# Kernel tuning notes

Hardware: AMD Instinct MI355X
Metric: run time of the kernel (lower is better)

The kernel has to match this reference:

```python
import jax, jax.numpy as jnp
import numpy as np

N_NODES = 100000
N_EDGES = 1600000
N_GRAPHS = 64
IN_DIM = 256
OUT_DIM = 512
H1 = OUT_DIM // 4   # 128
H2 = OUT_DIM // 2   # 256


def glorot(key, shape):
    lim = float(np.sqrt(6.0 / (shape[0] + shape[1])))
    return jax.random.uniform(key, shape, jnp.float32, -lim, lim)


def setup_inputs() -> dict:
    key = jax.random.key(0)
    ks = jax.random.split(key, 8)
    x = jax.random.normal(ks[0], (N_NODES, IN_DIM), jnp.float32)
    edge_index = jax.random.randint(ks[1], (2, N_EDGES), 0, N_NODES, jnp.int64)
    batch = jnp.sort(jax.random.randint(ks[2], (N_NODES,), 0, N_GRAPHS, jnp.int64))
    return {
        'x': x,
        'edge_index': edge_index,
        'batch': batch,
        'W1': glorot(ks[3], (IN_DIM, H1)),
        'b1': jnp.zeros((H1,), jnp.float32),
        'W2': glorot(ks[4], (H1, H2)),
        'b2': jnp.zeros((H2,), jnp.float32),
        'fc_W': glorot(ks[5], (H2, OUT_DIM)),
        'fc_b': jnp.zeros((OUT_DIM,), jnp.float32),
    }


def gcn_conv(x, W, b, src, dst, n_nodes):
    # PyG GCNConv (default): add self-loops, sym-normalized aggregation of XW + bias
    h = x @ W                                   # [N, F_out] transform first (cheaper gather)
    ones = jnp.ones((src.shape[0],), h.dtype)
    deg = jax.ops.segment_sum(ones, dst, num_segments=n_nodes)  # includes self-loops
    dinv = jax.lax.rsqrt(jnp.maximum(deg, 1.0))
    norm = dinv[src] * dinv[dst]                # [E]
    msg = h[src] * norm[:, None]                # gather + scale
    out = jax.ops.segment_sum(msg, dst, num_segments=n_nodes)   # scatter-add
    return out + b


def reference(x, edge_index, batch, W1, b1, W2, b2, fc_W, fc_b):
    n = x.shape[0]
    loops = jnp.arange(n, dtype=edge_index.dtype)
    src = jnp.concatenate([edge_index[0], loops])
    dst = jnp.concatenate([edge_index[1], loops])

    h = jax.nn.relu(gcn_conv(x, W1, b1, src, dst, n))   # dropout = identity (eval)
    h = jax.nn.relu(gcn_conv(h, W2, b2, src, dst, n))

    # global_mean_pool over batch ids
    sums = jax.ops.segment_sum(h, batch, num_segments=N_GRAPHS)
    cnts = jax.ops.segment_sum(jnp.ones((n,), h.dtype), batch, num_segments=N_GRAPHS)
    pooled = sums / jnp.maximum(cnts, 1.0)[:, None]     # [B, H2]

    return jax.nn.relu(pooled @ fc_W + fc_b)            # [B, OUT_DIM]
```

## Files before the change

### kernel.cpp

```cpp
#include <hip/hip_runtime.h>
#include <hip/hip_bf16.h>
#include <cstdint>

#define N_NODES 100000
#define N_EDGES 1600000
#define N_GRAPHS 64
#define IN_DIM 256
#define HD1 128
#define HD2 256
#define OUT_DIM 512

#define NBUCK 196
#define NBLK  196
#define EPB   8192

typedef __bf16 bf16x8 __attribute__((ext_vector_type(8)));
typedef float f32x4 __attribute__((ext_vector_type(4)));

static __device__ __forceinline__ float bflo(uint32_t v) { return __uint_as_float(v << 16); }
static __device__ __forceinline__ float bfhi(uint32_t v) { return __uint_as_float(v & 0xffff0000u); }
static __device__ __forceinline__ uint32_t f2bf_bits(float f) {
    uint32_t u = __float_as_uint(f);
    return (u + 0x7fffu + ((u >> 16) & 1u)) >> 16;
}
static __device__ __forceinline__ uint32_t packbf(float a, float b) {
    return f2bf_bits(a) | (f2bf_bits(b) << 16);
}
static __device__ __forceinline__ float bf2f(uint16_t b) { return __uint_as_float(((uint32_t)b) << 16); }

static __device__ __forceinline__ void gl_lds16(const void* g, void* l) {
    __builtin_amdgcn_global_load_lds((const __attribute__((address_space(1))) uint32_t*)g,
                                     (__attribute__((address_space(3))) uint32_t*)l, 16, 0, 0);
}

__global__ void k_probe(const uint32_t* __restrict__ xw, const int* __restrict__ ei,
                        int* __restrict__ flags) {
    if (threadIdx.x != 0 || blockIdx.x != 0) return;
    int mid = 0;
    for (int i = 0; i < 64; i++) {
        uint32_t f = (xw[i] >> 23) & 0xFF;
        if (f >= 64 && f < 200) mid++;
    }
    flags[0] = (mid < 32) ? 1 : 0;
    int nz = 0;
    for (int i = 0; i < 64; i++) if (ei[2 * i + 1] != 0) nz++;
    flags[1] = (nz == 0) ? 1 : 0;
}

static __device__ __forceinline__ int ld_idx(const int* p, int i, int sh) { return p[i << sh]; }
static __device__ __forceinline__ float ld_f(const void* p, int i, int isbf) {
    return isbf ? bf2f(((const uint16_t*)p)[i]) : ((const float*)p)[i];
}

__global__ __launch_bounds__(256) void k_prep(const void* __restrict__ W1, const void* __restrict__ W2,
                                              const void* __restrict__ fcW, const void* __restrict__ b1,
                                              const void* __restrict__ b2, const void* __restrict__ fcb,
                                              uint16_t* __restrict__ W1F, uint16_t* __restrict__ W2F,
                                              uint16_t* __restrict__ fcWc, uint16_t* __restrict__ bc1,
                                              uint16_t* __restrict__ bc2, uint16_t* __restrict__ fcbc,
                                              const int* __restrict__ flags) {
    int i = blockIdx.x * 256 + threadIdx.x;
    int isbf = flags[0];
    if (i < 32768) {
        int j = i & 7, l = (i >> 3) & 63, nt = (i >> 9) & 1, ks = (i >> 10) & 7, n0g = (i >> 13) & 3;
        int k = ks * 32 + (l >> 4) * 8 + j;
        int n = n0g * 32 + nt * 16 + (l & 15);
        W1F[i] = (uint16_t)f2bf_bits(ld_f(W1, k * HD1 + n, isbf));
    } else if (i < 65536) {
        int j2 = i - 32768;
        int j = j2 & 7, l = (j2 >> 3) & 63, nt = (j2 >> 9) & 1, ks = (j2 >> 10) & 3, n0g = (j2 >> 12) & 7;
        int k = ks * 32 + (l >> 4) * 8 + j;
        int n = n0g * 32 + nt * 16 + (l & 15);
        W2F[j2] = (uint16_t)f2bf_bits(ld_f(W2, k * HD2 + n, isbf));
    } else if (i < 196608) {
        int j = i - 65536;
        fcWc[j] = (uint16_t)f2bf_bits(ld_f(fcW, j, isbf));
    } else if (i < 196736) {
        bc1[i - 196608] = (uint16_t)f2bf_bits(ld_f(b1, i - 196608, isbf));
    } else if (i < 196992) {
        bc2[i - 196736] = (uint16_t)f2bf_bits(ld_f(b2, i - 196736, isbf));
    } else if (i < 197504) {
        fcbc[i - 196992] = (uint16_t)f2bf_bits(ld_f(fcb, i - 196992, isbf));
    }
}


__global__ __launch_bounds__(256) void k_hist(const int* __restrict__ ei, int* __restrict__ bh,
                                              const int* __restrict__ flags) {
    __shared__ int h[NBUCK];
    int t = threadIdx.x, blk = blockIdx.x;
    if (t < NBUCK) h[t] = 0;
    __syncthreads();
    int sh = flags[1];
    int base = blk * EPB;
#pragma unroll
    for (int k = 0; k < EPB / 256; k++) {
        int e = base + k * 256 + t;
        if (e < N_EDGES) atomicAdd(&h[ld_idx(ei, N_EDGES + e, sh) >> 9], 1);
    }
    __syncthreads();
    if (t < NBUCK) bh[blk * NBUCK + t] = h[t];
}

__global__ __launch_bounds__(256) void k_colscan(const int* __restrict__ bh, int* __restrict__ bhoff,
                                                 int* __restrict__ bucket_cnt) {
    __shared__ int s[256];
    int b = blockIdx.x, t = threadIdx.x;
    int v = (t < NBLK) ? bh[t * NBUCK + b] : 0;
    s[t] = v; __syncthreads();
    for (int off = 1; off < 256; off <<= 1) {
        int x = (t >= off) ? s[t - off] : 0;
        __syncthreads();
        s[t] += x;
        __syncthreads();
    }
    if (t < NBLK) bhoff[t * NBUCK + b] = s[t] - v;
    if (t == 255) bucket_cnt[b] = s[255];
}

__global__ __launch_bounds__(256) void k_bscan(const int* __restrict__ bucket_cnt,
                                               int* __restrict__ bucket_base,
                                               int* __restrict__ row_ptr) {
    __shared__ int s[256];
    int t = threadIdx.x;
    int v = (t < NBUCK) ? bucket_cnt[t] : 0;
    s[t] = v; __syncthreads();
    for (int off = 1; off < 256; off <<= 1) {
        int x = (t >= off) ? s[t - off] : 0;
        __syncthreads();
        s[t] += x;
        __syncthreads();
    }
    if (t < NBUCK) bucket_base[t] = s[t] - v;
    if (t == NBUCK - 1) { bucket_base[NBUCK] = s[t]; row_ptr[N_NODES] = s[t]; }
}

__global__ __launch_bounds__(256) void k_part(const int* __restrict__ ei,
                                              const int* __restrict__ bucket_base,
                                              const int* __restrict__ bhoff,
                                              int* __restrict__ tmp,
                                              const int* __restrict__ flags) {
    __shared__ int cur[NBUCK];
    int t = threadIdx.x, blk = blockIdx.x;
    if (t < NBUCK) cur[t] = bucket_base[t] + bhoff[blk * NBUCK + t];
    __syncthreads();
    int sh = flags[1];
    int base = blk * EPB;
#pragma unroll
    for (int k = 0; k < EPB / 256; k++) {
        int e = base + k * 256 + t;
        if (e < N_EDGES) {
            int s = ld_idx(ei, e, sh), d = ld_idx(ei, N_EDGES + e, sh);
            int pos = atomicAdd(&cur[d >> 9], 1);
            tmp[pos] = (s << 9) | (d & 511);
        }
    }
}

__global__ __launch_bounds__(256) void k_bsort(const int* __restrict__ tmp,
                                               const int* __restrict__ bucket_base,
                                               int* __restrict__ csr_src,
                                               int* __restrict__ row_ptr,
                                               float* __restrict__ dinv) {
    __shared__ int h[512], a[512], c[512];
    int b = blockIdx.x, t = threadIdx.x;
    int beg = bucket_base[b], end = bucket_base[b + 1];
    h[t] = 0; h[t + 256] = 0;
    __syncthreads();
    for (int i = beg + t; i < end; i += 256) atomicAdd(&h[tmp[i] & 511], 1);
    __syncthreads();
    a[t] = h[t]; a[t + 256] = h[t + 256];
    __syncthreads();
    for (int off = 1; off < 512; off <<= 1) {
        int x0 = (t >= off) ? a[t - off] : 0;
        int x1 = ((t + 256) >= off) ? a[t + 256 - off] : 0;
        __syncthreads();
        a[t] += x0; a[t + 256] += x1;
        __syncthreads();
    }
#pragma unroll
    for (int u = 0; u < 2; u++) {
        int i = t + u * 256;
        int node = (b << 9) + i;
        int ex = a[i] - h[i];
        if (node < N_NODES) {
            row_ptr[node] = beg + ex;
            dinv[node] = rsqrtf((float)(h[i] + 1));
        }
        c[i] = ex;
    }
    __syncthreads();
    for (int i = beg + t; i < end; i += 256) {
        int e = tmp[i];
        int pos = atomicAdd(&c[e & 511], 1);
        csr_src[beg + pos] = e >> 9;
    }
}

#define GCNT_CHUNK 8
__global__ __launch_bounds__(256) void k_gcnt(const int* __restrict__ bat, int* __restrict__ gcnt,
                                              const int* __restrict__ flags) {
    __shared__ int h[N_GRAPHS];
    int t = threadIdx.x;
    if (t < N_GRAPHS) h[t] = 0;
    __syncthreads();
    int sh = flags[1];
    int base = (blockIdx.x * 256 + t) * GCNT_CHUNK;
    int cur = -1, run = 0;
#pragma unroll
    for (int u = 0; u < GCNT_CHUNK; u++) {
        int i = base + u;
        if (i < N_NODES) {
            int g = ld_idx(bat, i, sh);
            if (g == cur) run++;
            else { if (run) atomicAdd(&h[cur], run); cur = g; run = 1; }
        }
    }
    if (run) atomicAdd(&h[cur], run);
    __syncthreads();
    if (t < N_GRAPHS) { int v = h[t]; if (v) atomicAdd(&gcnt[t], v); }
}


__global__ __launch_bounds__(256) void k_gemm1(const void* __restrict__ Ain,
                                               const uint16_t* __restrict__ BF,
                                               uint16_t* __restrict__ C,
                                               const int* __restrict__ flags) {
    __shared__ __align__(16) uint16_t As[64 * 256];
    const int M = N_NODES, N = HD1;
    int isbf = flags[0];
    int t = threadIdx.x;
    int wave = t >> 6, lane = t & 63;
    int quad = lane >> 4, l16 = lane & 15;
    int m0 = blockIdx.x * 64;
    int n0 = wave * 32;

    bf16x8 Bf[8][2];
#pragma unroll
    for (int ks = 0; ks < 8; ks++)
#pragma unroll
        for (int nt = 0; nt < 2; nt++)
            Bf[ks][nt] = *(const bf16x8*)(BF + ((((wave * 8 + ks) * 2 + nt) << 6) + lane) * 8);

    if (isbf) {
        const uint8_t* Xb = (const uint8_t*)Ain;
#pragma unroll
        for (int i = 0; i < 8; i++) {
            int o = (i * 256 + t) * 16;
            int r = o >> 9, c = o & 511;
            int rg = m0 + r; if (rg >= M) rg = M - 1;
            gl_lds16(Xb + (size_t)rg * 512 + (c ^ ((r & 7) << 4)), (uint8_t*)As + o);
        }
    } else {
        const float* Xf = (const float*)Ain;
#pragma unroll
        for (int i = 0; i < 8; i++) {
            int o = (i * 256 + t) * 16;
            int r = o >> 9, c = (o & 511) ^ ((r & 7) << 4);
            int rg = m0 + r; if (rg >= M) rg = M - 1;
            const float* p = Xf + (size_t)rg * 256 + (c >> 1);
            f32x4 f0 = *(const f32x4*)p, f1 = *(const f32x4*)(p + 4);
            union { uint16_t u[8]; bf16x8 v; } rr;
#pragma unroll
            for (int j = 0; j < 4; j++) {
                rr.u[j]     = (uint16_t)f2bf_bits(f0[j]);
                rr.u[4 + j] = (uint16_t)f2bf_bits(f1[j]);
            }
            *(bf16x8*)((uint8_t*)As + o) = rr.v;
        }
    }
    __syncthreads();

    f32x4 acc[4][2];
#pragma unroll
    for (int a = 0; a < 4; a++)
#pragma unroll
        for (int b = 0; b < 2; b++) acc[a][b] = f32x4{0.f, 0.f, 0.f, 0.f};

#pragma unroll
    for (int ks = 0; ks < 8; ks++) {
        bf16x8 af[4];
#pragma unroll
        for (int mt = 0; mt < 4; mt++) {
            int r = mt * 16 + l16;
            int cb = (ks * 64 + quad * 16) ^ ((r & 7) << 4);
            af[mt] = *(const bf16x8*)((const uint8_t*)As + r * 512 + cb);
        }
#pragma unroll
        for (int mt = 0; mt < 4; mt++)
#pragma unroll
            for (int nt = 0; nt < 2; nt++)
                acc[mt][nt] = __builtin_amdgcn_mfma_f32_16x16x32_bf16(af[mt], Bf[ks][nt], acc[mt][nt], 0, 0, 0);
    }

#pragma unroll
    for (int mt = 0; mt < 4; mt++)
#pragma unroll
        for (int reg = 0; reg < 4; reg++) {
            int row = m0 + mt * 16 + quad * 4 + reg;
            if (row < M)
#pragma unroll
                for (int nt = 0; nt < 2; nt++)
                    C[row * N + n0 + nt * 16 + l16] = (uint16_t)f2bf_bits(acc[mt][nt][reg]);
        }
}


template <int WITH_BIAS_RELU>
__global__ __launch_bounds__(256) void k_agg(const uint16_t* __restrict__ Yin, uint16_t* __restrict__ Yout,
                                             const int* __restrict__ row_ptr, const int* __restrict__ csr_src,
                                             const float* __restrict__ dinv, const uint16_t* __restrict__ bias) {
    int node = blockIdx.x * 4 + (threadIdx.x >> 6);
    int l = threadIdx.x & 63;
    const uint32_t* Y32 = (const uint32_t*)Yin;

    float wd = dinv[node];
    uint32_t v = Y32[(size_t)node * 64 + l];
    float a0 = wd * bflo(v), a1 = wd * bfhi(v);

    int e0 = row_ptr[node], e1 = row_ptr[node + 1];
    for (int cb = e0; cb < e1; cb += 64) {
        int cnt = e1 - cb; if (cnt > 64) cnt = 64;
        int my_src = 0; uint32_t my_w = 0;
        if (l < cnt) { my_src = csr_src[cb + l]; my_w = __float_as_uint(dinv[my_src]); }
        int rounds = (cnt + 15) >> 4;
        for (int r = 0; r < rounds; r++) {
            int jb = r * 16;
            uint32_t vv[16];
#pragma unroll
            for (int t = 0; t < 16; t++) {
                int s = __builtin_amdgcn_readlane(my_src, jb + t);
                vv[t] = Y32[(size_t)s * 64 + l];
            }
#pragma unroll
            for (int t = 0; t < 16; t++) {
                float w = __uint_as_float(__builtin_amdgcn_readlane(my_w, jb + t));
                a0 += w * bflo(vv[t]);
                a1 += w * bfhi(vv[t]);
            }
        }
    }
    a0 *= wd; a1 *= wd;
    if (WITH_BIAS_RELU) {
        a0 = fmaxf(a0 + bf2f(bias[2 * l]), 0.f);
        a1 = fmaxf(a1 + bf2f(bias[2 * l + 1]), 0.f);
    }
    ((uint32_t*)Yout)[(size_t)node * 64 + l] = packbf(a0, a1);
}


__global__ __launch_bounds__(512) void k_gemm2_pool(const uint16_t* __restrict__ A,
                                                    const uint16_t* __restrict__ BF,
                                                    const uint16_t* __restrict__ bias,
                                                    const int* __restrict__ bat,
                                                    const int* __restrict__ flags,
                                                    float* __restrict__ pooled) {
    __shared__ __align__(16) uint16_t As[64 * 128];
    const int M = N_NODES;
    int t = threadIdx.x;
    int wave = t >> 6, lane = t & 63;
    int quad = lane >> 4, l16 = lane & 15;
    int m0 = blockIdx.x * 64;
    int n0 = wave * 32;

    bf16x8 Bf[4][2];
#pragma unroll
    for (int ks = 0; ks < 4; ks++)
#pragma unroll
        for (int nt = 0; nt < 2; nt++)
            Bf[ks][nt] = *(const bf16x8*)(BF + ((((wave * 4 + ks) * 2 + nt) << 6) + lane) * 8);

#pragma unroll
    for (int i = 0; i < 2; i++) {
        int o = (i * 512 + t) * 16;
        int r = o >> 8, c = o & 255;
        int rg = m0 + r; if (rg >= M) rg = M - 1;
        gl_lds16((const uint8_t*)A + (size_t)rg * 256 + (c ^ ((r & 7) << 4)), (uint8_t*)As + o);
    }
    __syncthreads();

    f32x4 acc[4][2];
#pragma unroll
    for (int a = 0; a < 4; a++)
#pragma unroll
        for (int b = 0; b < 2; b++) acc[a][b] = f32x4{0.f, 0.f, 0.f, 0.f};

#pragma unroll
    for (int ks = 0; ks < 4; ks++) {
        bf16x8 af[4];
#pragma unroll
        for (int mt = 0; mt < 4; mt++) {
            int r = mt * 16 + l16;
            int cb = (ks * 64 + quad * 16) ^ ((r & 7) << 4);
            af[mt] = *(const bf16x8*)((const uint8_t*)As + r * 256 + cb);
        }
#pragma unroll
        for (int mt = 0; mt < 4; mt++)
#pragma unroll
            for (int nt = 0; nt < 2; nt++)
                acc[mt][nt] = __builtin_amdgcn_mfma_f32_16x16x32_bf16(af[mt], Bf[ks][nt], acc[mt][nt], 0, 0, 0);
    }

    int sh = flags[1];
    float bv[2];
#pragma unroll
    for (int nt = 0; nt < 2; nt++) bv[nt] = bf2f(bias[n0 + nt * 16 + l16]);

    int last = m0 + 63 < M ? m0 + 63 : M - 1;
    int gfirst = ld_idx(bat, m0, sh);
    int glast  = ld_idx(bat, last, sh);
    if ((m0 + 63 < M) && gfirst == glast) {
#pragma unroll
        for (int nt = 0; nt < 2; nt++) {
            float s = 0.f;
#pragma unroll
            for (int mt = 0; mt < 4; mt++)
#pragma unroll
                for (int reg = 0; reg < 4; reg++)
                    s += fmaxf(acc[mt][nt][reg] + bv[nt], 0.f);
            s += __shfl_xor(s, 16);
            s += __shfl_xor(s, 32);
            if (quad == 0)
                atomicAdd(&pooled[gfirst * HD2 + n0 + nt * 16 + l16], s);
        }
    } else {
#pragma unroll
        for (int mt = 0; mt < 4; mt++) {
#pragma unroll
            for (int reg = 0; reg < 4; reg++) {
                int row = m0 + mt * 16 + quad * 4 + reg;
                if (row < M) {
                    int g = ld_idx(bat, row, sh);
#pragma unroll
                    for (int nt = 0; nt < 2; nt++)
                        atomicAdd(&pooled[g * HD2 + n0 + nt * 16 + l16],
                                  fmaxf(acc[mt][nt][reg] + bv[nt], 0.f));
                }
            }
        }
    }
}


__global__ __launch_bounds__(512) void k_final(const float* __restrict__ pooled, const int* __restrict__ gcnt,
                                               const uint16_t* __restrict__ fcWc, const uint16_t* __restrict__ fcbc,
                                               void* __restrict__ out, const int* __restrict__ flags) {
    __shared__ float pm[HD2];
    int g = blockIdx.x, t = threadIdx.x;
    if (t < HD2) pm[t] = pooled[g * HD2 + t] / fmaxf((float)gcnt[g], 1.0f);
    __syncthreads();
    float acc = bf2f(fcbc[t]);
    for (int k = 0; k < HD2; k++) acc = fmaf(pm[k], bf2f(fcWc[k * OUT_DIM + t]), acc);
    acc = fmaxf(acc, 0.f);
    if (flags[0]) ((uint16_t*)out)[g * OUT_DIM + t] = (uint16_t)f2bf_bits(acc);
    else          ((float*)out)[g * OUT_DIM + t] = acc;
}


extern "C" void kernel_launch(void* const* d_in, const int* in_sizes, int n_in,
                              void* d_out, int out_size, void* d_ws, size_t ws_size,
                              hipStream_t stream) {
    const void* x   = d_in[0];
    const int*  ei  = (const int*)d_in[1];
    const int*  bat = (const int*)d_in[2];
    const void* W1  = d_in[3];
    const void* b1  = d_in[4];
    const void* W2  = d_in[5];
    const void* b2  = d_in[6];
    const void* fcW = d_in[7];
    const void* fcb = d_in[8];

    char* ws = (char*)d_ws;
    size_t off = 0;
    auto alloc = [&](size_t bytes) -> void* {
        void* p = ws + off;
        off += (bytes + 255) & ~(size_t)255;
        return p;
    };
    uint16_t* buf0 = (uint16_t*)alloc((size_t)N_NODES * HD1 * 2);
    uint16_t* Hb   = (uint16_t*)alloc((size_t)N_NODES * HD1 * 2);
    int*   row_ptr = (int*)alloc((N_NODES + 1) * 4);
    int*   csr_src = (int*)alloc((size_t)N_EDGES * 4);
    int*   tmp     = (int*)alloc((size_t)N_EDGES * 4);
    int*   bh      = (int*)alloc(NBLK * NBUCK * 4);
    int*   bhoff   = (int*)alloc(NBLK * NBUCK * 4);
    int*   bucket_cnt  = (int*)alloc(NBUCK * 4);
    int*   bucket_base = (int*)alloc((NBUCK + 1) * 4);
    float* dinv    = (float*)alloc(N_NODES * 4);
    int*   gcnt    = (int*)alloc(N_GRAPHS * 4);
    float* pooled  = (float*)alloc(N_GRAPHS * HD2 * 4);
    uint16_t* W1T  = (uint16_t*)alloc(IN_DIM * HD1 * 2);
    uint16_t* W2T  = (uint16_t*)alloc(HD1 * HD2 * 2);
    uint16_t* bc1  = (uint16_t*)alloc(HD1 * 2);
    uint16_t* bc2  = (uint16_t*)alloc(HD2 * 2);
    uint16_t* fcWc = (uint16_t*)alloc(HD2 * OUT_DIM * 2);
    uint16_t* fcbc = (uint16_t*)alloc(OUT_DIM * 2);
    int*   flags   = (int*)alloc(64 * 4);

    uint16_t* Y1 = buf0;
    uint16_t* Zb = buf0;

    hipMemsetAsync(gcnt, 0, N_GRAPHS * 4, stream);
    hipMemsetAsync(pooled, 0, N_GRAPHS * HD2 * 4, stream);

    k_probe<<<1, 64, 0, stream>>>((const uint32_t*)x, ei, flags);

    k_prep<<<(197504 + 255) / 256, 256, 0, stream>>>(W1, W2, fcW, b1, b2, fcb,
                                                     W1T, W2T, fcWc, bc1, bc2, fcbc, flags);

    k_hist<<<NBLK, 256, 0, stream>>>(ei, bh, flags);
    k_colscan<<<NBUCK, 256, 0, stream>>>(bh, bhoff, bucket_cnt);
    k_bscan<<<1, 256, 0, stream>>>(bucket_cnt, bucket_base, row_ptr);
    k_part<<<NBLK, 256, 0, stream>>>(ei, bucket_base, bhoff, tmp, flags);
    k_bsort<<<NBUCK, 256, 0, stream>>>(tmp, bucket_base, csr_src, row_ptr, dinv);

    k_gcnt<<<(N_NODES + 256 * GCNT_CHUNK - 1) / (256 * GCNT_CHUNK), 256, 0, stream>>>(bat, gcnt, flags);

    k_gemm1<<<(N_NODES + 63) / 64, 256, 0, stream>>>(x, W1T, Y1, flags);
    k_agg<1><<<N_NODES / 4, 256, 0, stream>>>(Y1, Hb, row_ptr, csr_src, dinv, bc1);

    k_agg<0><<<N_NODES / 4, 256, 0, stream>>>(Hb, Zb, row_ptr, csr_src, dinv, nullptr);
    k_gemm2_pool<<<(N_NODES + 63) / 64, 512, 0, stream>>>(Zb, W2T, bc2, bat, flags, pooled);

    k_final<<<N_GRAPHS, 512, 0, stream>>>(pooled, gcnt, fcWc, fcbc, d_out, flags);
}
```

Baseline: 417.8 us.

## Pack source index and degree weight per edge; process four nodes per wave

Adds a pass that stores each CSR edge as an (src, dinv[src]) int2, so the aggregation kernels no longer do a dependent dinv gather per edge. The aggregation now has each wave loop over four nodes and read edges in groups of 8 through scalar (readfirstlane) loads instead of cooperative 64-lane loads plus readlane. This trims launch count and the index-load dependency chain. In exchange it adds an extra kernel, 12.8MB of extra edge traffic, and less memory-level parallelism per wave (8 outstanding gathers instead of 16).

```diff
diff --git a/kernel.cpp b/kernel.cpp
--- a/kernel.cpp
+++ b/kernel.cpp
@@ -197,6 +197,16 @@
     }
 }
 
+__global__ __launch_bounds__(256) void k_wpack(const int* __restrict__ csr_src,
+                                               const float* __restrict__ dinv,
+                                               int2* __restrict__ csr_sw) {
+    int e = blockIdx.x * 256 + threadIdx.x;
+    if (e < N_EDGES) {
+        int s = csr_src[e];
+        csr_sw[e] = make_int2(s, __float_as_int(dinv[s]));
+    }
+}
+
 #define GCNT_CHUNK 8
 __global__ __launch_bounds__(256) void k_gcnt(const int* __restrict__ bat, int* __restrict__ gcnt,
                                               const int* __restrict__ flags) {
@@ -308,44 +318,49 @@
 
 template <int WITH_BIAS_RELU>
 __global__ __launch_bounds__(256) void k_agg(const uint16_t* __restrict__ Yin, uint16_t* __restrict__ Yout,
-                                             const int* __restrict__ row_ptr, const int* __restrict__ csr_src,
+                                             const int* __restrict__ row_ptr, const int2* __restrict__ csr_sw,
                                              const float* __restrict__ dinv, const uint16_t* __restrict__ bias) {
-    int node = blockIdx.x * 4 + (threadIdx.x >> 6);
     int l = threadIdx.x & 63;
+    int wid = (blockIdx.x << 2) | (threadIdx.x >> 6);
     const uint32_t* Y32 = (const uint32_t*)Yin;
-
-    float wd = dinv[node];
-    uint32_t v = Y32[(size_t)node * 64 + l];
-    float a0 = wd * bflo(v), a1 = wd * bfhi(v);
-
-    int e0 = row_ptr[node], e1 = row_ptr[node + 1];
-    for (int cb = e0; cb < e1; cb += 64) {
-        int cnt = e1 - cb; if (cnt > 64) cnt = 64;
-        int my_src = 0; uint32_t my_w = 0;
-        if (l < cnt) { my_src = csr_src[cb + l]; my_w = __float_as_uint(dinv[my_src]); }
-        int rounds = (cnt + 15) >> 4;
-        for (int r = 0; r < rounds; r++) {
-            int jb = r * 16;
-            uint32_t vv[16];
-#pragma unroll
-            for (int t = 0; t < 16; t++) {
-                int s = __builtin_amdgcn_readlane(my_src, jb + t);
+    float b0 = 0.f, b1 = 0.f;
+    if (WITH_BIAS_RELU) { b0 = bf2f(bias[2 * l]); b1 = bf2f(bias[2 * l + 1]); }
+    int nbeg = __builtin_amdgcn_readfirstlane(wid * 4);
+
+#pragma unroll 1
+    for (int node = nbeg; node < nbeg + 4; node++) {
+        int e0 = __builtin_amdgcn_readfirstlane(row_ptr[node]);
+        int e1 = __builtin_amdgcn_readfirstlane(row_ptr[node + 1]);
+        float wd = dinv[node];
+        uint32_t v = Y32[(size_t)node * 64 + l];
+        float a0 = wd * bflo(v), a1 = wd * bfhi(v);
+
+        for (int e = e0; e < e1; e += 8) {
+            uint32_t vv[8];
+            float    ww[8];
+#pragma unroll
+            for (int t = 0; t < 8; t++) {
+                int idx = (e + t < e1) ? e + t : e1 - 1;
+                int2 sw = csr_sw[idx];
+                int   s = __builtin_amdgcn_readfirstlane(sw.x);
+                float w = __uint_as_float((uint32_t)__builtin_amdgcn_readfirstlane(sw.y));
+                ww[t] = (e + t < e1) ? w : 0.f;
                 vv[t] = Y32[(size_t)s * 64 + l];
             }
 #pragma unroll
-            for (int t = 0; t < 16; t++) {
-                float w = __uint_as_float(__builtin_amdgcn_readlane(my_w, jb + t));
-                a0 += w * bflo(vv[t]);
-                a1 += w * bfhi(vv[t]);
+            for (int t = 0; t < 8; t++) {
+                a0 += ww[t] * bflo(vv[t]);
+                a1 += ww[t] * bfhi(vv[t]);
             }
         }
-    }
-    a0 *= wd; a1 *= wd;
-    if (WITH_BIAS_RELU) {
-        a0 = fmaxf(a0 + bf2f(bias[2 * l]), 0.f);
-        a1 = fmaxf(a1 + bf2f(bias[2 * l + 1]), 0.f);
-    }
-    ((uint32_t*)Yout)[(size_t)node * 64 + l] = packbf(a0, a1);
+
+        a0 *= wd; a1 *= wd;
+        if (WITH_BIAS_RELU) {
+            a0 = fmaxf(a0 + b0, 0.f);
+            a1 = fmaxf(a1 + b1, 0.f);
+        }
+        ((uint32_t*)Yout)[(size_t)node * 64 + l] = packbf(a0, a1);
+    }
 }
 
 
@@ -481,6 +496,7 @@
     uint16_t* Hb   = (uint16_t*)alloc((size_t)N_NODES * HD1 * 2);
     int*   row_ptr = (int*)alloc((N_NODES + 1) * 4);
     int*   csr_src = (int*)alloc((size_t)N_EDGES * 4);
+    int2*  csr_sw  = (int2*)alloc((size_t)N_EDGES * 8);
     int*   tmp     = (int*)alloc((size_t)N_EDGES * 4);
     int*   bh      = (int*)alloc(NBLK * NBUCK * 4);
     int*   bhoff   = (int*)alloc(NBLK * NBUCK * 4);
@@ -513,13 +529,14 @@
     k_bscan<<<1, 256, 0, stream>>>(bucket_cnt, bucket_base, row_ptr);
     k_part<<<NBLK, 256, 0, stream>>>(ei, bucket_base, bhoff, tmp, flags);
     k_bsort<<<NBUCK, 256, 0, stream>>>(tmp, bucket_base, csr_src, row_ptr, dinv);
+    k_wpack<<<N_EDGES / 256, 256, 0, stream>>>(csr_src, dinv, csr_sw);
 
     k_gcnt<<<(N_NODES + 256 * GCNT_CHUNK - 1) / (256 * GCNT_CHUNK), 256, 0, stream>>>(bat, gcnt, flags);
 
     k_gemm1<<<(N_NODES + 63) / 64, 256, 0, stream>>>(x, W1T, Y1, flags);
-    k_agg<1><<<N_NODES / 4, 256, 0, stream>>>(Y1, Hb, row_ptr, csr_src, dinv, bc1);
-
-    k_agg<0><<<N_NODES / 4, 256, 0, stream>>>(Hb, Zb, row_ptr, csr_src, dinv, nullptr);
+    k_agg<1><<<N_NODES / 16, 256, 0, stream>>>(Y1, Hb, row_ptr, csr_sw, dinv, bc1);
+
+    k_agg<0><<<N_NODES / 16, 256, 0, stream>>>(Hb, Zb, row_ptr, csr_sw, dinv, nullptr);
     k_gemm2_pool<<<(N_NODES + 63) / 64, 512, 0, stream>>>(Zb, W2T, bc2, bat, flags, pooled);
 
     k_final<<<N_GRAPHS, 512, 0, stream>>>(pooled, gcnt, fcWc, fcbc, d_out, flags);
```

Result: slower. 438.7 us (+5.0%).

## Fuse second-layer neighbor aggregation into the GEMM2 pooling kernel

Applied to the files above, without the earlier changes.

The second sparse aggregation moves from a standalone kernel into k_gemm2_pool. Each wave gathers and normalizes neighbor rows for 8 nodes and writes the bf16 result straight into the swizzled LDS tile that feeds the MFMA GEMM. This removes one kernel launch and the write and re-read of the intermediate 100000x128 activation. In exchange, the GEMM block now spends its time on latency-bound gathers, with lower occupancy at 512 threads, and can no longer overlap the tile load asynchronously.

```diff
diff --git a/kernel.cpp b/kernel.cpp
--- a/kernel.cpp
+++ b/kernel.cpp
@@ -349,10 +349,13 @@
 }
 
 
-__global__ __launch_bounds__(512) void k_gemm2_pool(const uint16_t* __restrict__ A,
+__global__ __launch_bounds__(512) void k_gemm2_pool(const uint16_t* __restrict__ Hb,
                                                     const uint16_t* __restrict__ BF,
                                                     const uint16_t* __restrict__ bias,
                                                     const int* __restrict__ bat,
+                                                    const int* __restrict__ row_ptr,
+                                                    const int* __restrict__ csr_src,
+                                                    const float* __restrict__ dinv,
                                                     const int* __restrict__ flags,
                                                     float* __restrict__ pooled) {
     __shared__ __align__(16) uint16_t As[64 * 128];
@@ -370,12 +373,41 @@
         for (int nt = 0; nt < 2; nt++)
             Bf[ks][nt] = *(const bf16x8*)(BF + ((((wave * 4 + ks) * 2 + nt) << 6) + lane) * 8);
 
-#pragma unroll
-    for (int i = 0; i < 2; i++) {
-        int o = (i * 512 + t) * 16;
-        int r = o >> 8, c = o & 255;
-        int rg = m0 + r; if (rg >= M) rg = M - 1;
-        gl_lds16((const uint8_t*)A + (size_t)rg * 256 + (c ^ ((r & 7) << 4)), (uint8_t*)As + o);
+    const uint32_t* Y32 = (const uint32_t*)Hb;
+#pragma unroll 1
+    for (int u = 0; u < 8; u++) {
+        int node = m0 + wave * 8 + u;
+        float a0 = 0.f, a1 = 0.f;
+        if (node < M) {
+            float wd = dinv[node];
+            uint32_t v = Y32[(size_t)node * 64 + lane];
+            a0 = wd * bflo(v); a1 = wd * bfhi(v);
+            int e0 = row_ptr[node], e1 = row_ptr[node + 1];
+            for (int cb = e0; cb < e1; cb += 64) {
+                int cnt = e1 - cb; if (cnt > 64) cnt = 64;
+                int my_src = 0; uint32_t my_w = 0;
+                if (lane < cnt) { my_src = csr_src[cb + lane]; my_w = __float_as_uint(dinv[my_src]); }
+                int rounds = (cnt + 15) >> 4;
+                for (int r = 0; r < rounds; r++) {
+                    int jb = r * 16;
+                    uint32_t vv[16];
+#pragma unroll
+                    for (int t2 = 0; t2 < 16; t2++) {
+                        int s = __builtin_amdgcn_readlane(my_src, jb + t2);
+                        vv[t2] = Y32[(size_t)s * 64 + lane];
+                    }
+#pragma unroll
+                    for (int t2 = 0; t2 < 16; t2++) {
+                        float w = __uint_as_float(__builtin_amdgcn_readlane(my_w, jb + t2));
+                        a0 += w * bflo(vv[t2]);
+                        a1 += w * bfhi(vv[t2]);
+                    }
+                }
+            }
+            a0 *= wd; a1 *= wd;
+        }
+        int r = wave * 8 + u;
+        ((uint32_t*)As)[r * 64 + (lane ^ ((r & 7) << 2))] = packbf(a0, a1);
     }
     __syncthreads();
 
@@ -477,7 +509,7 @@
         off += (bytes + 255) & ~(size_t)255;
         return p;
     };
-    uint16_t* buf0 = (uint16_t*)alloc((size_t)N_NODES * HD1 * 2);
+    uint16_t* Y1   = (uint16_t*)alloc((size_t)N_NODES * HD1 * 2);
     uint16_t* Hb   = (uint16_t*)alloc((size_t)N_NODES * HD1 * 2);
     int*   row_ptr = (int*)alloc((N_NODES + 1) * 4);
     int*   csr_src = (int*)alloc((size_t)N_EDGES * 4);
@@ -497,9 +529,6 @@
     uint16_t* fcbc = (uint16_t*)alloc(OUT_DIM * 2);
     int*   flags   = (int*)alloc(64 * 4);
 
-    uint16_t* Y1 = buf0;
-    uint16_t* Zb = buf0;
-
     hipMemsetAsync(gcnt, 0, N_GRAPHS * 4, stream);
     hipMemsetAsync(pooled, 0, N_GRAPHS * HD2 * 4, stream);
 
@@ -519,8 +548,8 @@
     k_gemm1<<<(N_NODES + 63) / 64, 256, 0, stream>>>(x, W1T, Y1, flags);
     k_agg<1><<<N_NODES / 4, 256, 0, stream>>>(Y1, Hb, row_ptr, csr_src, dinv, bc1);
 
-    k_agg<0><<<N_NODES / 4, 256, 0, stream>>>(Hb, Zb, row_ptr, csr_src, dinv, nullptr);
-    k_gemm2_pool<<<(N_NODES + 63) / 64, 512, 0, stream>>>(Zb, W2T, bc2, bat, flags, pooled);
+    k_gemm2_pool<<<(N_NODES + 63) / 64, 512, 0, stream>>>(Hb, W2T, bc2, bat,
+                                                          row_ptr, csr_src, dinv, flags, pooled);
 
     k_final<<<N_GRAPHS, 512, 0, stream>>>(pooled, gcnt, fcWc, fcbc, d_out, flags);
 }
```

After: 419.4 us. Within noise of the previous version (+0.4%).

## Merge independent prep, histogram, bucket sort, gemm1 and graph-count kernels via block-range dispatch

Applied to the files above, without the earlier changes.

Independent kernels are fused into combined launches that dispatch on block index: weight prep with the edge histogram, and bucket sort, the first GEMM and graph counting into one kernel. This removes launch gaps and lets independent work overlap on the GPU instead of serialising. The cost is that the merged kernel uses the GEMM's larger LDS footprint and register pressure for every block, which may reduce occupancy for the lighter sort and count blocks.

```diff
diff --git a/kernel.cpp b/kernel.cpp
--- a/kernel.cpp
+++ b/kernel.cpp
@@ -14,6 +14,11 @@
 #define NBLK  196
 #define EPB   8192
 
+#define GB1   1563
+#define GCNT_CHUNK 8
+#define GCNT_BLKS 49
+#define PREP_BLKS 772
+
 typedef __bf16 bf16x8 __attribute__((ext_vector_type(8)));
 typedef float f32x4 __attribute__((ext_vector_type(4)));
 
@@ -52,55 +57,55 @@
     return isbf ? bf2f(((const uint16_t*)p)[i]) : ((const float*)p)[i];
 }
 
-__global__ __launch_bounds__(256) void k_prep(const void* __restrict__ W1, const void* __restrict__ W2,
-                                              const void* __restrict__ fcW, const void* __restrict__ b1,
-                                              const void* __restrict__ b2, const void* __restrict__ fcb,
-                                              uint16_t* __restrict__ W1F, uint16_t* __restrict__ W2F,
-                                              uint16_t* __restrict__ fcWc, uint16_t* __restrict__ bc1,
-                                              uint16_t* __restrict__ bc2, uint16_t* __restrict__ fcbc,
-                                              const int* __restrict__ flags) {
-    int i = blockIdx.x * 256 + threadIdx.x;
-    int isbf = flags[0];
-    if (i < 32768) {
-        int j = i & 7, l = (i >> 3) & 63, nt = (i >> 9) & 1, ks = (i >> 10) & 7, n0g = (i >> 13) & 3;
-        int k = ks * 32 + (l >> 4) * 8 + j;
-        int n = n0g * 32 + nt * 16 + (l & 15);
-        W1F[i] = (uint16_t)f2bf_bits(ld_f(W1, k * HD1 + n, isbf));
-    } else if (i < 65536) {
-        int j2 = i - 32768;
-        int j = j2 & 7, l = (j2 >> 3) & 63, nt = (j2 >> 9) & 1, ks = (j2 >> 10) & 3, n0g = (j2 >> 12) & 7;
-        int k = ks * 32 + (l >> 4) * 8 + j;
-        int n = n0g * 32 + nt * 16 + (l & 15);
-        W2F[j2] = (uint16_t)f2bf_bits(ld_f(W2, k * HD2 + n, isbf));
-    } else if (i < 196608) {
-        int j = i - 65536;
-        fcWc[j] = (uint16_t)f2bf_bits(ld_f(fcW, j, isbf));
-    } else if (i < 196736) {
-        bc1[i - 196608] = (uint16_t)f2bf_bits(ld_f(b1, i - 196608, isbf));
-    } else if (i < 196992) {
-        bc2[i - 196736] = (uint16_t)f2bf_bits(ld_f(b2, i - 196736, isbf));
-    } else if (i < 197504) {
-        fcbc[i - 196992] = (uint16_t)f2bf_bits(ld_f(fcb, i - 196992, isbf));
-    }
-}
-
-
-__global__ __launch_bounds__(256) void k_hist(const int* __restrict__ ei, int* __restrict__ bh,
-                                              const int* __restrict__ flags) {
+__global__ __launch_bounds__(256) void k_prep_hist(const void* __restrict__ W1, const void* __restrict__ W2,
+                                                   const void* __restrict__ fcW, const void* __restrict__ b1,
+                                                   const void* __restrict__ b2, const void* __restrict__ fcb,
+                                                   uint16_t* __restrict__ W1F, uint16_t* __restrict__ W2F,
+                                                   uint16_t* __restrict__ fcWc, uint16_t* __restrict__ bc1,
+                                                   uint16_t* __restrict__ bc2, uint16_t* __restrict__ fcbc,
+                                                   const int* __restrict__ ei, int* __restrict__ bh,
+                                                   const int* __restrict__ flags) {
     __shared__ int h[NBUCK];
-    int t = threadIdx.x, blk = blockIdx.x;
-    if (t < NBUCK) h[t] = 0;
-    __syncthreads();
-    int sh = flags[1];
-    int base = blk * EPB;
-#pragma unroll
-    for (int k = 0; k < EPB / 256; k++) {
-        int e = base + k * 256 + t;
-        if (e < N_EDGES) atomicAdd(&h[ld_idx(ei, N_EDGES + e, sh) >> 9], 1);
-    }
-    __syncthreads();
-    if (t < NBUCK) bh[blk * NBUCK + t] = h[t];
-}
+    if (blockIdx.x < PREP_BLKS) {
+        int i = blockIdx.x * 256 + threadIdx.x;
+        int isbf = flags[0];
+        if (i < 32768) {
+            int j = i & 7, l = (i >> 3) & 63, nt = (i >> 9) & 1, ks = (i >> 10) & 7, n0g = (i >> 13) & 3;
+            int k = ks * 32 + (l >> 4) * 8 + j;
+            int n = n0g * 32 + nt * 16 + (l & 15);
+            W1F[i] = (uint16_t)f2bf_bits(ld_f(W1, k * HD1 + n, isbf));
+        } else if (i < 65536) {
+            int j2 = i - 32768;
+            int j = j2 & 7, l = (j2 >> 3) & 63, nt = (j2 >> 9) & 1, ks = (j2 >> 10) & 3, n0g = (j2 >> 12) & 7;
+            int k = ks * 32 + (l >> 4) * 8 + j;
+            int n = n0g * 32 + nt * 16 + (l & 15);
+            W2F[j2] = (uint16_t)f2bf_bits(ld_f(W2, k * HD2 + n, isbf));
+        } else if (i < 196608) {
+            int j = i - 65536;
+            fcWc[j] = (uint16_t)f2bf_bits(ld_f(fcW, j, isbf));
+        } else if (i < 196736) {
+            bc1[i - 196608] = (uint16_t)f2bf_bits(ld_f(b1, i - 196608, isbf));
+        } else if (i < 196992) {
+            bc2[i - 196736] = (uint16_t)f2bf_bits(ld_f(b2, i - 196736, isbf));
+        } else if (i < 197504) {
+            fcbc[i - 196992] = (uint16_t)f2bf_bits(ld_f(fcb, i - 196992, isbf));
+        }
+    } else {
+        int t = threadIdx.x, blk = blockIdx.x - PREP_BLKS;
+        if (t < NBUCK) h[t] = 0;
+        __syncthreads();
+        int sh = flags[1];
+        int base = blk * EPB;
+#pragma unroll
+        for (int k = 0; k < EPB / 256; k++) {
+            int e = base + k * 256 + t;
+            if (e < N_EDGES) atomicAdd(&h[ld_idx(ei, N_EDGES + e, sh) >> 9], 1);
+        }
+        __syncthreads();
+        if (t < NBUCK) bh[blk * NBUCK + t] = h[t];
+    }
+}
+
 
 __global__ __launch_bounds__(256) void k_colscan(const int* __restrict__ bh, int* __restrict__ bhoff,
                                                  int* __restrict__ bucket_cnt) {
@@ -157,152 +162,154 @@
     }
 }
 
-__global__ __launch_bounds__(256) void k_bsort(const int* __restrict__ tmp,
-                                               const int* __restrict__ bucket_base,
-                                               int* __restrict__ csr_src,
-                                               int* __restrict__ row_ptr,
-                                               float* __restrict__ dinv) {
-    __shared__ int h[512], a[512], c[512];
-    int b = blockIdx.x, t = threadIdx.x;
-    int beg = bucket_base[b], end = bucket_base[b + 1];
-    h[t] = 0; h[t + 256] = 0;
-    __syncthreads();
-    for (int i = beg + t; i < end; i += 256) atomicAdd(&h[tmp[i] & 511], 1);
-    __syncthreads();
-    a[t] = h[t]; a[t + 256] = h[t + 256];
-    __syncthreads();
-    for (int off = 1; off < 512; off <<= 1) {
-        int x0 = (t >= off) ? a[t - off] : 0;
-        int x1 = ((t + 256) >= off) ? a[t + 256 - off] : 0;
-        __syncthreads();
-        a[t] += x0; a[t + 256] += x1;
-        __syncthreads();
-    }
-#pragma unroll
-    for (int u = 0; u < 2; u++) {
-        int i = t + u * 256;
-        int node = (b << 9) + i;
-        int ex = a[i] - h[i];
-        if (node < N_NODES) {
-            row_ptr[node] = beg + ex;
-            dinv[node] = rsqrtf((float)(h[i] + 1));
-        }
-        c[i] = ex;
-    }
-    __syncthreads();
-    for (int i = beg + t; i < end; i += 256) {
-        int e = tmp[i];
-        int pos = atomicAdd(&c[e & 511], 1);
-        csr_src[beg + pos] = e >> 9;
-    }
-}
-
-#define GCNT_CHUNK 8
-__global__ __launch_bounds__(256) void k_gcnt(const int* __restrict__ bat, int* __restrict__ gcnt,
-                                              const int* __restrict__ flags) {
-    __shared__ int h[N_GRAPHS];
-    int t = threadIdx.x;
-    if (t < N_GRAPHS) h[t] = 0;
-    __syncthreads();
-    int sh = flags[1];
-    int base = (blockIdx.x * 256 + t) * GCNT_CHUNK;
-    int cur = -1, run = 0;
-#pragma unroll
-    for (int u = 0; u < GCNT_CHUNK; u++) {
-        int i = base + u;
-        if (i < N_NODES) {
-            int g = ld_idx(bat, i, sh);
-            if (g == cur) run++;
-            else { if (run) atomicAdd(&h[cur], run); cur = g; run = 1; }
-        }
-    }
-    if (run) atomicAdd(&h[cur], run);
-    __syncthreads();
-    if (t < N_GRAPHS) { int v = h[t]; if (v) atomicAdd(&gcnt[t], v); }
-}
-
-
-__global__ __launch_bounds__(256) void k_gemm1(const void* __restrict__ Ain,
-                                               const uint16_t* __restrict__ BF,
-                                               uint16_t* __restrict__ C,
-                                               const int* __restrict__ flags) {
-    __shared__ __align__(16) uint16_t As[64 * 256];
-    const int M = N_NODES, N = HD1;
-    int isbf = flags[0];
-    int t = threadIdx.x;
-    int wave = t >> 6, lane = t & 63;
-    int quad = lane >> 4, l16 = lane & 15;
-    int m0 = blockIdx.x * 64;
-    int n0 = wave * 32;
-
-    bf16x8 Bf[8][2];
-#pragma unroll
-    for (int ks = 0; ks < 8; ks++)
-#pragma unroll
-        for (int nt = 0; nt < 2; nt++)
-            Bf[ks][nt] = *(const bf16x8*)(BF + ((((wave * 8 + ks) * 2 + nt) << 6) + lane) * 8);
-
-    if (isbf) {
-        const uint8_t* Xb = (const uint8_t*)Ain;
-#pragma unroll
-        for (int i = 0; i < 8; i++) {
-            int o = (i * 256 + t) * 16;
-            int r = o >> 9, c = o & 511;
-            int rg = m0 + r; if (rg >= M) rg = M - 1;
-            gl_lds16(Xb + (size_t)rg * 512 + (c ^ ((r & 7) << 4)), (uint8_t*)As + o);
-        }
+__global__ __launch_bounds__(256) void k_merge1(const int* __restrict__ tmp,
+                                                const int* __restrict__ bucket_base,
+                                                int* __restrict__ csr_src,
+                                                int* __restrict__ row_ptr,
+                                                float* __restrict__ dinv,
+                                                const void* __restrict__ Ain,
+                                                const uint16_t* __restrict__ BF,
+                                                uint16_t* __restrict__ C,
+                                                const int* __restrict__ bat,
+                                                int* __restrict__ gcnt,
+                                                const int* __restrict__ flags) {
+    __shared__ __align__(16) uint8_t lds[64 * 256 * 2];
+    int bx = blockIdx.x;
+    if (bx < NBUCK) {
+        int* h = (int*)lds; int* a = h + 512; int* c = a + 512;
+        int b = bx, t = threadIdx.x;
+        int beg = bucket_base[b], end = bucket_base[b + 1];
+        h[t] = 0; h[t + 256] = 0;
+        __syncthreads();
+        for (int i = beg + t; i < end; i += 256) atomicAdd(&h[tmp[i] & 511], 1);
+        __syncthreads();
+        a[t] = h[t]; a[t + 256] = h[t + 256];
+        __syncthreads();
+        for (int off = 1; off < 512; off <<= 1) {
+            int x0 = (t >= off) ? a[t - off] : 0;
+            int x1 = ((t + 256) >= off) ? a[t + 256 - off] : 0;
+            __syncthreads();
+            a[t] += x0; a[t + 256] += x1;
+            __syncthreads();
+        }
+#pragma unroll
+        for (int u = 0; u < 2; u++) {
+            int i = t + u * 256;
+            int node = (b << 9) + i;
+            int ex = a[i] - h[i];
+            if (node < N_NODES) {
+                row_ptr[node] = beg + ex;
+                dinv[node] = rsqrtf((float)(h[i] + 1));
+            }
+            c[i] = ex;
+        }
+        __syncthreads();
+        for (int i = beg + t; i < end; i += 256) {
+            int e = tmp[i];
+            int pos = atomicAdd(&c[e & 511], 1);
+            csr_src[beg + pos] = e >> 9;
+        }
+    } else if (bx < NBUCK + GB1) {
+        uint16_t* As = (uint16_t*)lds;
+        const int M = N_NODES, N = HD1;
+        int isbf = flags[0];
+        int t = threadIdx.x;
+        int wave = t >> 6, lane = t & 63;
+        int quad = lane >> 4, l16 = lane & 15;
+        int bid = bx - NBUCK;
+        int m0 = bid * 64;
+        int n0 = wave * 32;
+
+        bf16x8 Bf[8][2];
+#pragma unroll
+        for (int ks = 0; ks < 8; ks++)
+#pragma unroll
+            for (int nt = 0; nt < 2; nt++)
+                Bf[ks][nt] = *(const bf16x8*)(BF + ((((wave * 8 + ks) * 2 + nt) << 6) + lane) * 8);
+
+        if (isbf) {
+            const uint8_t* Xb = (const uint8_t*)Ain;
+#pragma unroll
+            for (int i = 0; i < 8; i++) {
+                int o = (i * 256 + t) * 16;
+                int r = o >> 9, c = o & 511;
+                int rg = m0 + r; if (rg >= M) rg = M - 1;
+                gl_lds16(Xb + (size_t)rg * 512 + (c ^ ((r & 7) << 4)), (uint8_t*)As + o);
+            }
+        } else {
+            const float* Xf = (const float*)Ain;
+#pragma unroll
+            for (int i = 0; i < 8; i++) {
+                int o = (i * 256 + t) * 16;
+                int r = o >> 9, c = (o & 511) ^ ((r & 7) << 4);
+                int rg = m0 + r; if (rg >= M) rg = M - 1;
+                const float* p = Xf + (size_t)rg * 256 + (c >> 1);
+                f32x4 f0 = *(const f32x4*)p, f1 = *(const f32x4*)(p + 4);
+                union { uint16_t u[8]; bf16x8 v; } rr;
+#pragma unroll
+                for (int j = 0; j < 4; j++) {
+                    rr.u[j]     = (uint16_t)f2bf_bits(f0[j]);
+                    rr.u[4 + j] = (uint16_t)f2bf_bits(f1[j]);
+                }
+                *(bf16x8*)((uint8_t*)As + o) = rr.v;
+            }
+        }
+        __syncthreads();
+
+        f32x4 acc[4][2];
+#pragma unroll
+        for (int a = 0; a < 4; a++)
+#pragma unroll
+            for (int b = 0; b < 2; b++) acc[a][b] = f32x4{0.f, 0.f, 0.f, 0.f};
+
+#pragma unroll
+        for (int ks = 0; ks < 8; ks++) {
+            bf16x8 af[4];
+#pragma unroll
+            for (int mt = 0; mt < 4; mt++) {
+                int r = mt * 16 + l16;
+                int cb = (ks * 64 + quad * 16) ^ ((r & 7) << 4);
+                af[mt] = *(const bf16x8*)((const uint8_t*)As + r * 512 + cb);
+            }
+#pragma unroll
+            for (int mt = 0; mt < 4; mt++)
+#pragma unroll
+                for (int nt = 0; nt < 2; nt++)
+                    acc[mt][nt] = __builtin_amdgcn_mfma_f32_16x16x32_bf16(af[mt], Bf[ks][nt], acc[mt][nt], 0, 0, 0);
+        }
+
+#pragma unroll
+        for (int mt = 0; mt < 4; mt++)
+#pragma unroll
+            for (int reg = 0; reg < 4; reg++) {
+                int row = m0 + mt * 16 + quad * 4 + reg;
+                if (row < M)
+#pragma unroll
+                    for (int nt = 0; nt < 2; nt++)
+                        C[row * N + n0 + nt * 16 + l16] = (uint16_t)f2bf_bits(acc[mt][nt][reg]);
+            }
     } else {
-        const float* Xf = (const float*)Ain;
-#pragma unroll
-        for (int i = 0; i < 8; i++) {
-            int o = (i * 256 + t) * 16;
-            int r = o >> 9, c = (o & 511) ^ ((r & 7) << 4);
-            int rg = m0 + r; if (rg >= M) rg = M - 1;
-            const float* p = Xf + (size_t)rg * 256 + (c >> 1);
-            f32x4 f0 = *(const f32x4*)p, f1 = *(const f32x4*)(p + 4);
-            union { uint16_t u[8]; bf16x8 v; } rr;
-#pragma unroll
-            for (int j = 0; j < 4; j++) {
-                rr.u[j]     = (uint16_t)f2bf_bits(f0[j]);
-                rr.u[4 + j] = (uint16_t)f2bf_bits(f1[j]);
-            }
-            *(bf16x8*)((uint8_t*)As + o) = rr.v;
-        }
-    }
-    __syncthreads();
-
-    f32x4 acc[4][2];
-#pragma unroll
-    for (int a = 0; a < 4; a++)
-#pragma unroll
-        for (int b = 0; b < 2; b++) acc[a][b] = f32x4{0.f, 0.f, 0.f, 0.f};
-
-#pragma unroll
-    for (int ks = 0; ks < 8; ks++) {
-        bf16x8 af[4];
-#pragma unroll
-        for (int mt = 0; mt < 4; mt++) {
-            int r = mt * 16 + l16;
-            int cb = (ks * 64 + quad * 16) ^ ((r & 7) << 4);
-            af[mt] = *(const bf16x8*)((const uint8_t*)As + r * 512 + cb);
-        }
-#pragma unroll
-        for (int mt = 0; mt < 4; mt++)
-#pragma unroll
-            for (int nt = 0; nt < 2; nt++)
-                acc[mt][nt] = __builtin_amdgcn_mfma_f32_16x16x32_bf16(af[mt], Bf[ks][nt], acc[mt][nt], 0, 0, 0);
-    }
-
-#pragma unroll
-    for (int mt = 0; mt < 4; mt++)
-#pragma unroll
-        for (int reg = 0; reg < 4; reg++) {
-            int row = m0 + mt * 16 + quad * 4 + reg;
-            if (row < M)
-#pragma unroll
-                for (int nt = 0; nt < 2; nt++)
-                    C[row * N + n0 + nt * 16 + l16] = (uint16_t)f2bf_bits(acc[mt][nt][reg]);
-        }
+        int* h = (int*)lds;
+        int t = threadIdx.x;
+        if (t < N_GRAPHS) h[t] = 0;
+        __syncthreads();
+        int sh = flags[1];
+        int blk = bx - NBUCK - GB1;
+        int base = (blk * 256 + t) * GCNT_CHUNK;
+        int cur = -1, run = 0;
+#pragma unroll
+        for (int u = 0; u < GCNT_CHUNK; u++) {
+            int i = base + u;
+            if (i < N_NODES) {
+                int g = ld_idx(bat, i, sh);
+                if (g == cur) run++;
+                else { if (run) atomicAdd(&h[cur], run); cur = g; run = 1; }
+            }
+        }
+        if (run) atomicAdd(&h[cur], run);
+        __syncthreads();
+        if (t < N_GRAPHS) { int v = h[t]; if (v) atomicAdd(&gcnt[t], v); }
+    }
 }
 
 
@@ -505,18 +512,17 @@
 
     k_probe<<<1, 64, 0, stream>>>((const uint32_t*)x, ei, flags);
 
-    k_prep<<<(197504 + 255) / 256, 256, 0, stream>>>(W1, W2, fcW, b1, b2, fcb,
-                                                     W1T, W2T, fcWc, bc1, bc2, fcbc, flags);
-
-    k_hist<<<NBLK, 256, 0, stream>>>(ei, bh, flags);
+    k_prep_hist<<<PREP_BLKS + NBLK, 256, 0, stream>>>(W1, W2, fcW, b1, b2, fcb,
+                                                      W1T, W2T, fcWc, bc1, bc2, fcbc,
+                                                      ei, bh, flags);
+
     k_colscan<<<NBUCK, 256, 0, stream>>>(bh, bhoff, bucket_cnt);
     k_bscan<<<1, 256, 0, stream>>>(bucket_cnt, bucket_base, row_ptr);
     k_part<<<NBLK, 256, 0, stream>>>(ei, bucket_base, bhoff, tmp, flags);
-    k_bsort<<<NBUCK, 256, 0, stream>>>(tmp, bucket_base, csr_src, row_ptr, dinv);
-
-    k_gcnt<<<(N_NODES + 256 * GCNT_CHUNK - 1) / (256 * GCNT_CHUNK), 256, 0, stream>>>(bat, gcnt, flags);
-
-    k_gemm1<<<(N_NODES + 63) / 64, 256, 0, stream>>>(x, W1T, Y1, flags);
+
+    k_merge1<<<NBUCK + GB1 + GCNT_BLKS, 256, 0, stream>>>(tmp, bucket_base, csr_src, row_ptr, dinv,
+                                                          x, W1T, Y1, bat, gcnt, flags);
+
     k_agg<1><<<N_NODES / 4, 256, 0, stream>>>(Y1, Hb, row_ptr, csr_src, dinv, bc1);
 
     k_agg<0><<<N_NODES / 4, 256, 0, stream>>>(Hb, Zb, row_ptr, csr_src, dinv, nullptr);
```

Measured after the change: 400.6 us. 4.1% less time.
